# Kernel optimization log

Hardware: AMD Instinct MI355X
Metric: run time of the kernel (lower is better)

The kernel has to match this reference:

```python
import jax, jax.numpy as jnp
import numpy as np

B, S, D, H = 4, 2048, 768, 12
DK = D // H

def setup_inputs() -> dict:
    key = jax.random.key(0)
    ks = jax.random.split(key, 9)
    s = 0.02
    return {
        "z": jax.random.normal(ks[0], (B, S, D), dtype=jnp.float32),
        "wq_w": jax.random.normal(ks[1], (D, D), dtype=jnp.float32) * s,
        "wq_b": jnp.zeros((D,), dtype=jnp.float32),
        "wk_w": jax.random.normal(ks[2], (D, D), dtype=jnp.float32) * s,
        "wk_b": jnp.zeros((D,), dtype=jnp.float32),
        "wv_w": jax.random.normal(ks[3], (D, D), dtype=jnp.float32) * s,
        "wv_b": jnp.zeros((D,), dtype=jnp.float32),
        "fc_w": jax.random.normal(ks[4], (D, D), dtype=jnp.float32) * s,
        "fc_b": jnp.zeros((D,), dtype=jnp.float32),
    }

def reference(z, wq_w, wq_b, wk_w, wk_b, wv_w, wv_b, fc_w, fc_b):
    # Dropout layers are treated as eval-mode (identity), as is standard for
    # a deterministic correctness baseline.
    b, s, d = z.shape
    temp = jnp.asarray(DK ** 0.5, dtype=z.dtype)
    # QKV projections -> [b, h, s, dk]
    def proj(w, bias):
        return (z @ w.T + bias).reshape(b, s, H, DK).transpose(0, 2, 1, 3)
    q = proj(wq_w, wq_b)
    k = proj(wk_w, wk_b)
    v = proj(wv_w, wv_b)
    # raw attention weights (pre-softmax), as returned by ScaleDotAttention
    attn_weights = jnp.einsum('bhqd,bhkd->bhqk', q / temp, k)  # [b,h,s,s]
    attn_probs = jax.nn.softmax(attn_weights, axis=-1)
    context = jnp.einsum('bhqk,bhkd->bhqd', attn_probs, v)  # [b,h,s,dk]
    avg_weights = jnp.sum(attn_weights, axis=1) / H  # [b,s,s]
    context = context.transpose(0, 2, 1, 3).reshape(b, s, d)
    attn_output = context @ fc_w.T + fc_b
    return attn_output, avg_weights
```

## Files before the change

kernel.cpp:

```cpp
#include <hip/hip_runtime.h>
#include <hip/hip_fp16.h>

#define Bc 4
#define Sc 2048
#define Dc 768
#define Hc 12
#define DKc 64

typedef _Float16 f16;
typedef __attribute__((ext_vector_type(8))) _Float16 f16x8;
typedef __attribute__((ext_vector_type(4))) _Float16 f16x4;
typedef __attribute__((ext_vector_type(4))) float f32x4;

static __device__ __forceinline__ f32x4 mfma16(f16x8 a, f16x8 b, f32x4 c) {
  return __builtin_amdgcn_mfma_f32_16x16x32_f16(a, b, c, 0, 0, 0);
}

#define GLD16(g, l)                                              \
  __builtin_amdgcn_global_load_lds(                              \
      (const __attribute__((address_space(1))) void*)(g),        \
      (__attribute__((address_space(3))) void*)(l), 16, 0, 0)

__global__ __launch_bounds__(256) void cvt_f32_f16(const float* __restrict__ in,
                                                   f16* __restrict__ out, int n4) {
  int i = blockIdx.x * blockDim.x + threadIdx.x;
  if (i >= n4) return;
  float4 v = reinterpret_cast<const float4*>(in)[i];
  f16x4 o;
  o[0] = (f16)v.x; o[1] = (f16)v.y; o[2] = (f16)v.z; o[3] = (f16)v.w;
  reinterpret_cast<f16x4*>(out)[i] = o;
}

template <int MODE>
__global__ __launch_bounds__(256) void gemm128(
    const f16* __restrict__ A, const f16* __restrict__ Bw,
    const float* __restrict__ bias, void* __restrict__ dst,
    int M, int N, int K, long sAz, long sBz, long sDz, float scale) {
  const int tid  = threadIdx.x;
  const int lane = tid & 63;
  const int w    = tid >> 6;
  const int wr = w >> 1, wc = w & 1;
  const int l15 = lane & 15, lg = lane >> 4;
  const long m0 = (long)blockIdx.x * 128;
  const long n0 = (long)blockIdx.y * 128;
  const f16* Ab = A + (long)blockIdx.z * sAz + m0 * K;
  const f16* Bb = Bw + (long)blockIdx.z * sBz + n0 * K;

  __shared__ f16 As[128][32];
  __shared__ f16 Bs[128][32];

  f32x4 acc[4][4] = {};

  const int srow = lane >> 2;
  const int scol = (lane & 3) * 8;
  const f16* Ag = Ab + (long)(w * 32 + srow) * K + scol;
  const f16* Bg = Bb + (long)(w * 32 + srow) * K + scol;
  f16* As0 = &As[w * 32][0];
  f16* As1 = &As[w * 32 + 16][0];
  f16* Bs0 = &Bs[w * 32][0];
  f16* Bs1 = &Bs[w * 32 + 16][0];
  const long k16 = (long)16 * K;

  for (int k0 = 0; k0 < K; k0 += 32) {
    GLD16(Ag + k0, As0);
    GLD16(Ag + k0 + k16, As1);
    GLD16(Bg + k0, Bs0);
    GLD16(Bg + k0 + k16, Bs1);
    __syncthreads();
    f16x8 af[4], bf[4];
#pragma unroll
    for (int i = 0; i < 4; ++i) {
      af[i] = *reinterpret_cast<const f16x8*>(&As[wr * 64 + i * 16 + l15][lg * 8]);
      bf[i] = *reinterpret_cast<const f16x8*>(&Bs[wc * 64 + i * 16 + l15][lg * 8]);
    }
#pragma unroll
    for (int mi = 0; mi < 4; ++mi)
#pragma unroll
      for (int ni = 0; ni < 4; ++ni)
        acc[mi][ni] = mfma16(af[mi], bf[ni], acc[mi][ni]);
    __syncthreads();
  }

#pragma unroll
  for (int mi = 0; mi < 4; ++mi) {
#pragma unroll
    for (int ni = 0; ni < 4; ++ni) {
      const long col = n0 + wc * 64 + ni * 16 + l15;
      const float bv = (MODE == 3) ? 0.0f : bias[col];
#pragma unroll
      for (int j = 0; j < 4; ++j) {
        const long row = m0 + wr * 64 + mi * 16 + lg * 4 + j;
        float val = acc[mi][ni][j] + bv;
        if (MODE == 0) {
          ((f16*)dst)[row * N + col] = (f16)val;
        } else if (MODE == 1) {
          const long b = row >> 11, s = row & 2047;
          ((f16*)dst)[(b * N + col) * (long)Sc + s] = (f16)val;
        } else if (MODE == 2) {
          ((float*)dst)[row * N + col] = val;
        } else {
          float* dp = (float*)dst + (long)blockIdx.z * sDz;
          dp[row * N + col] = val * scale;
        }
      }
    }
  }
}

__global__ __launch_bounds__(512) void attn8(const f16* __restrict__ Q,
                                             const f16* __restrict__ Km,
                                             const f16* __restrict__ Vt,
                                             f16* __restrict__ ctx) {
  const int tid = threadIdx.x;
  const int lane = tid & 63;
  const int w = tid >> 6;
  const int l15 = lane & 15, lg = lane >> 4;
  const int bid = blockIdx.x;
  const int qt = bid & 15;
  const int h  = (bid >> 4) % Hc;
  const int b  = bid / (16 * Hc);
  const int q0 = qt * 128 + w * 16;

  __shared__ f16 Ks[64][72];
  __shared__ f16 Vs[64][72];
  __shared__ f16 Ps[8][16][72];

  f16x8 qf[2];
  {
    const f16* qp = Q + ((long)(b * Sc + q0 + l15)) * Dc + h * DKc + lg * 8;
    qf[0] = *reinterpret_cast<const f16x8*>(qp);
    qf[1] = *reinterpret_cast<const f16x8*>(qp + 32);
  }

  const int srow = tid >> 3;
  const int scol = (tid & 7) * 8;
  const f16* Kb = Km + (long)(b * Sc) * Dc + h * DKc;
  const f16* Vb = Vt + ((long)(b * Dc + h * DKc)) * Sc;

  const float c2 = 0.18033688011f;
  float m2 = -1e30f, l_run = 0.f;
  f32x4 o[4] = {};

  *reinterpret_cast<f16x8*>(&Ks[srow][scol]) =
      *reinterpret_cast<const f16x8*>(Kb + (long)srow * Dc + scol);
  *reinterpret_cast<f16x8*>(&Vs[srow][scol]) =
      *reinterpret_cast<const f16x8*>(Vb + (long)srow * Sc + scol);
  __syncthreads();

  for (int kv0 = 0; kv0 < Sc; kv0 += 64) {
    const bool pf = (kv0 + 64) < Sc;
    f16x8 kr, vr;
    if (pf) {
      kr = *reinterpret_cast<const f16x8*>(Kb + (long)(kv0 + 64 + srow) * Dc + scol);
      vr = *reinterpret_cast<const f16x8*>(Vb + (long)srow * Sc + kv0 + 64 + scol);
    }

    f32x4 sc[4];
    __builtin_amdgcn_s_setprio(1);
#pragma unroll
    for (int t = 0; t < 4; ++t) {
      f32x4 s = {};
      s = mfma16(*reinterpret_cast<const f16x8*>(&Ks[t * 16 + l15][lg * 8]), qf[0], s);
      s = mfma16(*reinterpret_cast<const f16x8*>(&Ks[t * 16 + l15][32 + lg * 8]), qf[1], s);
      sc[t] = s;
    }
    __builtin_amdgcn_s_setprio(0);

    float mx = sc[0][0];
#pragma unroll
    for (int t = 0; t < 4; ++t)
#pragma unroll
      for (int j = 0; j < 4; ++j) mx = fmaxf(mx, sc[t][j]);
    const float mx2 = mx * c2;
    float al = 1.0f;
    if (!__all(mx2 <= m2 + 11.544f)) {
      float g = fmaxf(mx2, __shfl_xor(mx2, 16));
      g = fmaxf(g, __shfl_xor(g, 32));
      const float mn2 = fmaxf(m2, g);
      al = __builtin_amdgcn_exp2f(m2 - mn2);
      m2 = mn2;
#pragma unroll
      for (int c = 0; c < 4; ++c)
#pragma unroll
        for (int j = 0; j < 4; ++j) o[c][j] *= al;
    }
    float ps = 0.f;
    f16x4 pp[4];
#pragma unroll
    for (int t = 0; t < 4; ++t)
#pragma unroll
      for (int j = 0; j < 4; ++j) {
        float p = __builtin_amdgcn_exp2f(__builtin_fmaf(sc[t][j], c2, -m2));
        pp[t][j] = (f16)p;
        ps += p;
      }
    ps += __shfl_xor(ps, 16);
    ps += __shfl_xor(ps, 32);
    l_run = l_run * al + ps;

#pragma unroll
    for (int t = 0; t < 4; ++t)
      *reinterpret_cast<f16x4*>(&Ps[w][l15][t * 16 + lg * 4]) = pp[t];
    asm volatile("s_waitcnt lgkmcnt(0)" ::: "memory");
    __builtin_amdgcn_sched_barrier(0);

    f16x8 pa0 = *reinterpret_cast<const f16x8*>(&Ps[w][l15][lg * 8]);
    f16x8 pa1 = *reinterpret_cast<const f16x8*>(&Ps[w][l15][32 + lg * 8]);
    __builtin_amdgcn_s_setprio(1);
#pragma unroll
    for (int c = 0; c < 4; ++c) {
      o[c] = mfma16(*reinterpret_cast<const f16x8*>(&Vs[c * 16 + l15][lg * 8]), pa0, o[c]);
      o[c] = mfma16(*reinterpret_cast<const f16x8*>(&Vs[c * 16 + l15][32 + lg * 8]), pa1, o[c]);
    }
    __builtin_amdgcn_s_setprio(0);

    if (pf) {
      __syncthreads();
      *reinterpret_cast<f16x8*>(&Ks[srow][scol]) = kr;
      *reinterpret_cast<f16x8*>(&Vs[srow][scol]) = vr;
      __syncthreads();
    }
  }

  const float inv = 1.0f / l_run;
  f16* cp = ctx + ((long)(b * Sc) + q0 + l15) * Dc + h * DKc;
#pragma unroll
  for (int c = 0; c < 4; ++c) {
    f16x4 ov;
#pragma unroll
    for (int j = 0; j < 4; ++j) ov[j] = (f16)(o[c][j] * inv);
    *reinterpret_cast<f16x4*>(cp + c * 16 + lg * 4) = ov;
  }
}

extern "C" void kernel_launch(void* const* d_in, const int* in_sizes, int n_in,
                              void* d_out, int out_size, void* d_ws, size_t ws_size,
                              hipStream_t stream) {
  (void)in_sizes; (void)n_in; (void)out_size; (void)ws_size;
  const float* z    = (const float*)d_in[0];
  const float* wq_w = (const float*)d_in[1];
  const float* wq_b = (const float*)d_in[2];
  const float* wk_w = (const float*)d_in[3];
  const float* wk_b = (const float*)d_in[4];
  const float* wv_w = (const float*)d_in[5];
  const float* wv_b = (const float*)d_in[6];
  const float* fc_w = (const float*)d_in[7];
  const float* fc_b = (const float*)d_in[8];
  float* out = (float*)d_out;

  char* ws = (char*)d_ws;
  size_t off = 0;
  auto alloc = [&](size_t bytes) -> void* {
    void* p = (void*)(ws + off);
    off += (bytes + 255) & ~(size_t)255;
    return p;
  };
  const size_t zdb = (size_t)Bc * Sc * Dc * sizeof(f16);
  const size_t wdb = (size_t)Dc * Dc * sizeof(f16);
  f16* zb  = (f16*)alloc(zdb);
  f16* wqb = (f16*)alloc(wdb);
  f16* wkb = (f16*)alloc(wdb);
  f16* wvb = (f16*)alloc(wdb);
  f16* fcb = (f16*)alloc(wdb);
  f16* Qb  = (f16*)alloc(zdb);
  f16* Kb  = (f16*)alloc(zdb);
  f16* Vt  = (f16*)alloc(zdb);
  f16* Cx  = zb;

  const int nz4 = Bc * Sc * Dc / 4;
  const int nw4 = Dc * Dc / 4;
  cvt_f32_f16<<<nz4 / 256, 256, 0, stream>>>(z, zb, nz4);
  cvt_f32_f16<<<nw4 / 256, 256, 0, stream>>>(wq_w, wqb, nw4);
  cvt_f32_f16<<<nw4 / 256, 256, 0, stream>>>(wk_w, wkb, nw4);
  cvt_f32_f16<<<nw4 / 256, 256, 0, stream>>>(wv_w, wvb, nw4);
  cvt_f32_f16<<<nw4 / 256, 256, 0, stream>>>(fc_w, fcb, nw4);

  dim3 gproj(Bc * Sc / 128, Dc / 128, 1);
  gemm128<0><<<gproj, 256, 0, stream>>>(zb, wqb, wq_b, Qb, Bc * Sc, Dc, Dc, 0, 0, 0, 1.f);
  gemm128<0><<<gproj, 256, 0, stream>>>(zb, wkb, wk_b, Kb, Bc * Sc, Dc, Dc, 0, 0, 0, 1.f);
  gemm128<1><<<gproj, 256, 0, stream>>>(zb, wvb, wv_b, Vt, Bc * Sc, Dc, Dc, 0, 0, 0, 1.f);

  dim3 gavg(Sc / 128, Sc / 128, Bc);
  gemm128<3><<<gavg, 256, 0, stream>>>(Qb, Kb, nullptr, out + (size_t)Bc * Sc * Dc,
                                       Sc, Sc, Dc, (long)Sc * Dc, (long)Sc * Dc,
                                       (long)Sc * Sc, 1.0f / 96.0f);

  attn8<<<Bc * Hc * (Sc / 128), 512, 0, stream>>>(Qb, Kb, Vt, Cx);

  gemm128<2><<<gproj, 256, 0, stream>>>(Cx, fcb, fc_b, out, Bc * Sc, Dc, Dc, 0, 0, 0, 1.f);
}
```

Baseline: 246.6 us.

## Merge conversion and QKV launches, swizzle attention LDS, remap attention blocks

```diff
diff --git a/kernel.cpp b/kernel.cpp
--- a/kernel.cpp
+++ b/kernel.cpp
@@ -21,24 +21,110 @@
       (const __attribute__((address_space(1))) void*)(g),        \
       (__attribute__((address_space(3))) void*)(l), 16, 0, 0)
 
-__global__ __launch_bounds__(256) void cvt_f32_f16(const float* __restrict__ in,
-                                                   f16* __restrict__ out, int n4) {
-  int i = blockIdx.x * blockDim.x + threadIdx.x;
-  if (i >= n4) return;
+#define SWZ(row, colB) (((row) << 7) + ((colB) ^ (((row) & 7) << 4)))
+
+__global__ __launch_bounds__(256) void cvt5(
+    const float* __restrict__ z, const float* __restrict__ w0,
+    const float* __restrict__ w1, const float* __restrict__ w2,
+    const float* __restrict__ w3, f16* __restrict__ oz, f16* __restrict__ o0,
+    f16* __restrict__ o1, f16* __restrict__ o2, f16* __restrict__ o3) {
+  const int bid = blockIdx.x;
+  const float* in;
+  f16* out;
+  int i0;
+  if (bid < 6144)      { in = z;  out = oz; i0 = bid * 256; }
+  else if (bid < 6720) { in = w0; out = o0; i0 = (bid - 6144) * 256; }
+  else if (bid < 7296) { in = w1; out = o1; i0 = (bid - 6720) * 256; }
+  else if (bid < 7872) { in = w2; out = o2; i0 = (bid - 7296) * 256; }
+  else                 { in = w3; out = o3; i0 = (bid - 7872) * 256; }
+  const int i = i0 + threadIdx.x;
   float4 v = reinterpret_cast<const float4*>(in)[i];
   f16x4 o;
   o[0] = (f16)v.x; o[1] = (f16)v.y; o[2] = (f16)v.z; o[3] = (f16)v.w;
   reinterpret_cast<f16x4*>(out)[i] = o;
 }
 
+#define GEMM_CORE(Ab, Bb, K)                                                   \
+  __shared__ f16 As[128][32];                                                  \
+  __shared__ f16 Bs[128][32];                                                  \
+  f32x4 acc[4][4] = {};                                                        \
+  const int srow = lane >> 2;                                                  \
+  const int scol = (lane & 3) * 8;                                             \
+  const f16* Ag = (Ab) + (long)(w * 32 + srow) * (K) + scol;                   \
+  const f16* Bg = (Bb) + (long)(w * 32 + srow) * (K) + scol;                   \
+  f16* As0 = &As[w * 32][0];                                                   \
+  f16* As1 = &As[w * 32 + 16][0];                                              \
+  f16* Bs0 = &Bs[w * 32][0];                                                   \
+  f16* Bs1 = &Bs[w * 32 + 16][0];                                              \
+  const long k16 = (long)16 * (K);                                             \
+  for (int k0 = 0; k0 < (K); k0 += 32) {                                       \
+    GLD16(Ag + k0, As0);                                                       \
+    GLD16(Ag + k0 + k16, As1);                                                 \
+    GLD16(Bg + k0, Bs0);                                                       \
+    GLD16(Bg + k0 + k16, Bs1);                                                 \
+    __syncthreads();                                                           \
+    f16x8 af[4], bf[4];                                                        \
+    _Pragma("unroll") for (int i = 0; i < 4; ++i) {                            \
+      af[i] = *reinterpret_cast<const f16x8*>(&As[wr * 64 + i * 16 + l15][lg * 8]); \
+      bf[i] = *reinterpret_cast<const f16x8*>(&Bs[wc * 64 + i * 16 + l15][lg * 8]); \
+    }                                                                          \
+    _Pragma("unroll") for (int mi = 0; mi < 4; ++mi)                           \
+      _Pragma("unroll") for (int ni = 0; ni < 4; ++ni)                         \
+        acc[mi][ni] = mfma16(af[mi], bf[ni], acc[mi][ni]);                     \
+    __syncthreads();                                                           \
+  }
+
+__global__ __launch_bounds__(256) void gemm_qkv(
+    const f16* __restrict__ zb, const f16* __restrict__ wq,
+    const f16* __restrict__ wk, const f16* __restrict__ wv,
+    const float* __restrict__ bq, const float* __restrict__ bk,
+    const float* __restrict__ bv, f16* __restrict__ Qb, f16* __restrict__ Kb,
+    f16* __restrict__ Vt) {
+  const int tid = threadIdx.x;
+  const int lane = tid & 63;
+  const int w = tid >> 6;
+  const int wr = w >> 1, wc = w & 1;
+  const int l15 = lane & 15, lg = lane >> 4;
+  const int sel = blockIdx.y / 6;
+  const long m0 = (long)blockIdx.x * 128;
+  const long n0 = (long)(blockIdx.y % 6) * 128;
+  const f16* Bw = sel == 0 ? wq : sel == 1 ? wk : wv;
+  const float* bias = sel == 0 ? bq : sel == 1 ? bk : bv;
+  const f16* Ab = zb + m0 * Dc;
+  const f16* Bb = Bw + n0 * Dc;
+
+  GEMM_CORE(Ab, Bb, Dc)
+
+  f16* dq = sel == 0 ? Qb : Kb;
+#pragma unroll
+  for (int mi = 0; mi < 4; ++mi) {
+#pragma unroll
+    for (int ni = 0; ni < 4; ++ni) {
+      const long col = n0 + wc * 64 + ni * 16 + l15;
+      const float bv2 = bias[col];
+#pragma unroll
+      for (int j = 0; j < 4; ++j) {
+        const long row = m0 + wr * 64 + mi * 16 + lg * 4 + j;
+        const float val = acc[mi][ni][j] + bv2;
+        if (sel < 2) {
+          dq[row * Dc + col] = (f16)val;
+        } else {
+          const long b = row >> 11, s = row & 2047;
+          Vt[(b * Dc + col) * (long)Sc + s] = (f16)val;
+        }
+      }
+    }
+  }
+}
+
 template <int MODE>
 __global__ __launch_bounds__(256) void gemm128(
     const f16* __restrict__ A, const f16* __restrict__ Bw,
-    const float* __restrict__ bias, void* __restrict__ dst,
-    int M, int N, int K, long sAz, long sBz, long sDz, float scale) {
-  const int tid  = threadIdx.x;
+    const float* __restrict__ bias, float* __restrict__ dst,
+    int N, int K, long sAz, long sBz, long sDz, float scale) {
+  const int tid = threadIdx.x;
   const int lane = tid & 63;
-  const int w    = tid >> 6;
+  const int w = tid >> 6;
   const int wr = w >> 1, wc = w & 1;
   const int l15 = lane & 15, lg = lane >> 4;
   const long m0 = (long)blockIdx.x * 128;
@@ -46,41 +132,9 @@
   const f16* Ab = A + (long)blockIdx.z * sAz + m0 * K;
   const f16* Bb = Bw + (long)blockIdx.z * sBz + n0 * K;
 
-  __shared__ f16 As[128][32];
-  __shared__ f16 Bs[128][32];
-
-  f32x4 acc[4][4] = {};
-
-  const int srow = lane >> 2;
-  const int scol = (lane & 3) * 8;
-  const f16* Ag = Ab + (long)(w * 32 + srow) * K + scol;
-  const f16* Bg = Bb + (long)(w * 32 + srow) * K + scol;
-  f16* As0 = &As[w * 32][0];
-  f16* As1 = &As[w * 32 + 16][0];
-  f16* Bs0 = &Bs[w * 32][0];
-  f16* Bs1 = &Bs[w * 32 + 16][0];
-  const long k16 = (long)16 * K;
-
-  for (int k0 = 0; k0 < K; k0 += 32) {
-    GLD16(Ag + k0, As0);
-    GLD16(Ag + k0 + k16, As1);
-    GLD16(Bg + k0, Bs0);
-    GLD16(Bg + k0 + k16, Bs1);
-    __syncthreads();
-    f16x8 af[4], bf[4];
-#pragma unroll
-    for (int i = 0; i < 4; ++i) {
-      af[i] = *reinterpret_cast<const f16x8*>(&As[wr * 64 + i * 16 + l15][lg * 8]);
-      bf[i] = *reinterpret_cast<const f16x8*>(&Bs[wc * 64 + i * 16 + l15][lg * 8]);
-    }
-#pragma unroll
-    for (int mi = 0; mi < 4; ++mi)
-#pragma unroll
-      for (int ni = 0; ni < 4; ++ni)
-        acc[mi][ni] = mfma16(af[mi], bf[ni], acc[mi][ni]);
-    __syncthreads();
-  }
-
+  GEMM_CORE(Ab, Bb, K)
+
+  float* dp = dst + (long)blockIdx.z * sDz;
 #pragma unroll
   for (int mi = 0; mi < 4; ++mi) {
 #pragma unroll
@@ -90,18 +144,8 @@
 #pragma unroll
       for (int j = 0; j < 4; ++j) {
         const long row = m0 + wr * 64 + mi * 16 + lg * 4 + j;
-        float val = acc[mi][ni][j] + bv;
-        if (MODE == 0) {
-          ((f16*)dst)[row * N + col] = (f16)val;
-        } else if (MODE == 1) {
-          const long b = row >> 11, s = row & 2047;
-          ((f16*)dst)[(b * N + col) * (long)Sc + s] = (f16)val;
-        } else if (MODE == 2) {
-          ((float*)dst)[row * N + col] = val;
-        } else {
-          float* dp = (float*)dst + (long)blockIdx.z * sDz;
-          dp[row * N + col] = val * scale;
-        }
+        const float val = acc[mi][ni][j] + bv;
+        dp[row * N + col] = (MODE == 3) ? val * scale : val;
       }
     }
   }
@@ -115,15 +159,18 @@
   const int lane = tid & 63;
   const int w = tid >> 6;
   const int l15 = lane & 15, lg = lane >> 4;
-  const int bid = blockIdx.x;
-  const int qt = bid & 15;
-  const int h  = (bid >> 4) % Hc;
-  const int b  = bid / (16 * Hc);
+  const int lid = (blockIdx.x & 7) * 96 + (blockIdx.x >> 3);
+  const int qt = lid & 15;
+  const int h  = (lid >> 4) % Hc;
+  const int b  = lid / (16 * Hc);
   const int q0 = qt * 128 + w * 16;
 
-  __shared__ f16 Ks[64][72];
-  __shared__ f16 Vs[64][72];
-  __shared__ f16 Ps[8][16][72];
+  __shared__ f16 Ks[64 * 64];
+  __shared__ f16 Vs[64 * 64];
+  __shared__ f16 Ps[8 * 16 * 64];
+  char* kb = (char*)Ks;
+  char* vb = (char*)Vs;
+  char* pb = (char*)Ps + (w << 11);
 
   f16x8 qf[2];
   {
@@ -133,35 +180,36 @@
   }
 
   const int srow = tid >> 3;
-  const int scol = (tid & 7) * 8;
-  const f16* Kb = Km + (long)(b * Sc) * Dc + h * DKc;
-  const f16* Vb = Vt + ((long)(b * Dc + h * DKc)) * Sc;
+  const int scolB = (tid & 7) * 16;
+  const f16* Kg = Km + (long)(b * Sc) * Dc + h * DKc;
+  const f16* Vg = Vt + ((long)(b * Dc + h * DKc)) * Sc;
 
   const float c2 = 0.18033688011f;
   float m2 = -1e30f, l_run = 0.f;
   f32x4 o[4] = {};
 
-  *reinterpret_cast<f16x8*>(&Ks[srow][scol]) =
-      *reinterpret_cast<const f16x8*>(Kb + (long)srow * Dc + scol);
-  *reinterpret_cast<f16x8*>(&Vs[srow][scol]) =
-      *reinterpret_cast<const f16x8*>(Vb + (long)srow * Sc + scol);
+  *reinterpret_cast<f16x8*>(kb + SWZ(srow, scolB)) =
+      *reinterpret_cast<const f16x8*>(Kg + (long)srow * Dc + scolB / 2);
+  *reinterpret_cast<f16x8*>(vb + SWZ(srow, scolB)) =
+      *reinterpret_cast<const f16x8*>(Vg + (long)srow * Sc + scolB / 2);
   __syncthreads();
 
   for (int kv0 = 0; kv0 < Sc; kv0 += 64) {
     const bool pf = (kv0 + 64) < Sc;
     f16x8 kr, vr;
     if (pf) {
-      kr = *reinterpret_cast<const f16x8*>(Kb + (long)(kv0 + 64 + srow) * Dc + scol);
-      vr = *reinterpret_cast<const f16x8*>(Vb + (long)srow * Sc + kv0 + 64 + scol);
+      kr = *reinterpret_cast<const f16x8*>(Kg + (long)(kv0 + 64 + srow) * Dc + scolB / 2);
+      vr = *reinterpret_cast<const f16x8*>(Vg + (long)srow * Sc + kv0 + 64 + scolB / 2);
     }
 
     f32x4 sc[4];
     __builtin_amdgcn_s_setprio(1);
 #pragma unroll
     for (int t = 0; t < 4; ++t) {
+      const int row = t * 16 + l15;
       f32x4 s = {};
-      s = mfma16(*reinterpret_cast<const f16x8*>(&Ks[t * 16 + l15][lg * 8]), qf[0], s);
-      s = mfma16(*reinterpret_cast<const f16x8*>(&Ks[t * 16 + l15][32 + lg * 8]), qf[1], s);
+      s = mfma16(*reinterpret_cast<const f16x8*>(kb + SWZ(row, lg * 16)), qf[0], s);
+      s = mfma16(*reinterpret_cast<const f16x8*>(kb + SWZ(row, 64 + lg * 16)), qf[1], s);
       sc[t] = s;
     }
     __builtin_amdgcn_s_setprio(0);
@@ -200,24 +248,25 @@
 
 #pragma unroll
     for (int t = 0; t < 4; ++t)
-      *reinterpret_cast<f16x4*>(&Ps[w][l15][t * 16 + lg * 4]) = pp[t];
+      *reinterpret_cast<f16x4*>(pb + SWZ(l15, t * 32 + lg * 8)) = pp[t];
     asm volatile("s_waitcnt lgkmcnt(0)" ::: "memory");
     __builtin_amdgcn_sched_barrier(0);
 
-    f16x8 pa0 = *reinterpret_cast<const f16x8*>(&Ps[w][l15][lg * 8]);
-    f16x8 pa1 = *reinterpret_cast<const f16x8*>(&Ps[w][l15][32 + lg * 8]);
+    f16x8 pa0 = *reinterpret_cast<const f16x8*>(pb + SWZ(l15, lg * 16));
+    f16x8 pa1 = *reinterpret_cast<const f16x8*>(pb + SWZ(l15, 64 + lg * 16));
     __builtin_amdgcn_s_setprio(1);
 #pragma unroll
     for (int c = 0; c < 4; ++c) {
-      o[c] = mfma16(*reinterpret_cast<const f16x8*>(&Vs[c * 16 + l15][lg * 8]), pa0, o[c]);
-      o[c] = mfma16(*reinterpret_cast<const f16x8*>(&Vs[c * 16 + l15][32 + lg * 8]), pa1, o[c]);
+      const int row = c * 16 + l15;
+      o[c] = mfma16(*reinterpret_cast<const f16x8*>(vb + SWZ(row, lg * 16)), pa0, o[c]);
+      o[c] = mfma16(*reinterpret_cast<const f16x8*>(vb + SWZ(row, 64 + lg * 16)), pa1, o[c]);
     }
     __builtin_amdgcn_s_setprio(0);
 
     if (pf) {
       __syncthreads();
-      *reinterpret_cast<f16x8*>(&Ks[srow][scol]) = kr;
-      *reinterpret_cast<f16x8*>(&Vs[srow][scol]) = vr;
+      *reinterpret_cast<f16x8*>(kb + SWZ(srow, scolB)) = kr;
+      *reinterpret_cast<f16x8*>(vb + SWZ(srow, scolB)) = vr;
       __syncthreads();
     }
   }
@@ -267,25 +316,18 @@
   f16* Vt  = (f16*)alloc(zdb);
   f16* Cx  = zb;
 
-  const int nz4 = Bc * Sc * Dc / 4;
-  const int nw4 = Dc * Dc / 4;
-  cvt_f32_f16<<<nz4 / 256, 256, 0, stream>>>(z, zb, nz4);
-  cvt_f32_f16<<<nw4 / 256, 256, 0, stream>>>(wq_w, wqb, nw4);
-  cvt_f32_f16<<<nw4 / 256, 256, 0, stream>>>(wk_w, wkb, nw4);
-  cvt_f32_f16<<<nw4 / 256, 256, 0, stream>>>(wv_w, wvb, nw4);
-  cvt_f32_f16<<<nw4 / 256, 256, 0, stream>>>(fc_w, fcb, nw4);
-
-  dim3 gproj(Bc * Sc / 128, Dc / 128, 1);
-  gemm128<0><<<gproj, 256, 0, stream>>>(zb, wqb, wq_b, Qb, Bc * Sc, Dc, Dc, 0, 0, 0, 1.f);
-  gemm128<0><<<gproj, 256, 0, stream>>>(zb, wkb, wk_b, Kb, Bc * Sc, Dc, Dc, 0, 0, 0, 1.f);
-  gemm128<1><<<gproj, 256, 0, stream>>>(zb, wvb, wv_b, Vt, Bc * Sc, Dc, Dc, 0, 0, 0, 1.f);
+  cvt5<<<8448, 256, 0, stream>>>(z, wq_w, wk_w, wv_w, fc_w, zb, wqb, wkb, wvb, fcb);
+
+  dim3 gqkv(Bc * Sc / 128, 18, 1);
+  gemm_qkv<<<gqkv, 256, 0, stream>>>(zb, wqb, wkb, wvb, wq_b, wk_b, wv_b, Qb, Kb, Vt);
 
   dim3 gavg(Sc / 128, Sc / 128, Bc);
   gemm128<3><<<gavg, 256, 0, stream>>>(Qb, Kb, nullptr, out + (size_t)Bc * Sc * Dc,
-                                       Sc, Sc, Dc, (long)Sc * Dc, (long)Sc * Dc,
+                                       Sc, Dc, (long)Sc * Dc, (long)Sc * Dc,
                                        (long)Sc * Sc, 1.0f / 96.0f);
 
   attn8<<<Bc * Hc * (Sc / 128), 512, 0, stream>>>(Qb, Kb, Vt, Cx);
 
-  gemm128<2><<<gproj, 256, 0, stream>>>(Cx, fcb, fc_b, out, Bc * Sc, Dc, Dc, 0, 0, 0, 1.f);
-}
+  dim3 gfc(Bc * Sc / 128, Dc / 128, 1);
+  gemm128<2><<<gfc, 256, 0, stream>>>(Cx, fcb, fc_b, out, Dc, Dc, 0, 0, 0, 1.f);
+}
```

New measurement: 221.8 us. -10.0%, faster.
